# Optimization experiments

Measured on AMD Instinct MI355X. Metric: run time of the kernel, lower is better.

## Reference

```python
import jax, jax.numpy as jnp
import numpy as np

ALPHA = 0.25
GAMMA = 2.0
VAR0, VAR1 = 0.1, 0.2  # torch.Tensor([0.1, 0.2]) variances in encode
EPS = 1e-4


def _center_size(boxes):
    # corner (x1,y1,x2,y2) -> center (cx,cy,w,h)
    return jnp.concatenate([(boxes[:, :2] + boxes[:, 2:]) * 0.5,
                            boxes[:, 2:] - boxes[:, :2]], axis=1)


def _jaccard(a, b):
    # a: [A,4] anchors, b: [T,4] targets, corner form -> IoU [A,T]
    lt = jnp.maximum(a[:, None, :2], b[None, :, :2])
    rb = jnp.minimum(a[:, None, 2:], b[None, :, 2:])
    wh = jnp.clip(rb - lt, 0.0)
    inter = wh[..., 0] * wh[..., 1]
    area_a = (a[:, 2] - a[:, 0]) * (a[:, 3] - a[:, 1])
    area_b = (b[:, 2] - b[:, 0]) * (b[:, 3] - b[:, 1])
    return inter / (area_a[:, None] + area_b[None, :] - inter)


def _encode(matched, priors_cf):
    # matched: corner form [P,4]; priors_cf: center form [P,4]
    g_cxcy = ((matched[:, :2] + matched[:, 2:]) * 0.5 - priors_cf[:, :2]) / (VAR0 * priors_cf[:, 2:])
    g_wh = jnp.log((matched[:, 2:] - matched[:, :2]) / priors_cf[:, 2:]) / VAR1
    return jnp.concatenate([g_cxcy, g_wh], axis=1)


def _per_image(cla, reg, target, anchor, anchor_cf):
    # cla [A,C], reg [A,4], target [T,5]
    valid = target[:, 4] != -1.0                      # padded targets (label -1) are excluded
    has_valid = jnp.any(valid)
    cla = jnp.clip(cla, EPS, 1.0 - EPS)
    iou = _jaccard(anchor, target[:, :4])             # [A,T]
    iou = jnp.where(valid[None, :], iou, -1.0)        # mask padded targets (valid IoUs are >= 0)
    iou_argmax = jnp.argmax(iou, axis=1)              # [A]
    iou_max = jnp.take_along_axis(iou, iou_argmax[:, None], axis=1)[:, 0]
    pos = iou_max >= 0.5
    num_pos = jnp.sum(pos)
    assigned = target[iou_argmax]                     # [A,5] gather of matched gt

    C = cla.shape[1]
    onehot = jax.nn.one_hot(assigned[:, 4].astype(jnp.int32), C, dtype=cla.dtype)
    labels = jnp.full_like(cla, -1.0)
    labels = jnp.where(iou_max[:, None] < 0.4, 0.0, labels)
    labels = jnp.where(pos[:, None], onehot, labels)

    is_one = labels == 1.0
    alpha_factor = jnp.where(is_one, ALPHA, 1.0 - ALPHA)
    focal_weight = alpha_factor * jnp.where(is_one, 1.0 - cla, cla) ** GAMMA
    bce = -(labels * jnp.log(cla) + (1.0 - labels) * jnp.log1p(-cla))
    cls_loss = jnp.where(labels != -1.0, focal_weight * bce, 0.0)
    cls_loss = cls_loss.sum() / jnp.maximum(num_pos.astype(cla.dtype), 1.0)

    # smooth-L1 on positive anchors only; original takes .mean() over [P,4]
    enc_gt = _encode(assigned[:, :4], anchor_cf)      # [A,4]
    diff = jnp.abs(enc_gt - reg)
    sl1 = jnp.where(diff <= 1.0 / 9.0, 0.5 * 9.0 * diff * diff, diff - 0.5 / 9.0)
    denom = jnp.maximum(num_pos * 4, 1).astype(cla.dtype)
    reg_loss = jnp.where(num_pos > 0, jnp.sum(sl1 * pos[:, None]) / denom, 0.0)

    cls_loss = jnp.where(has_valid, cls_loss, 0.0)
    reg_loss = jnp.where(has_valid, reg_loss, 0.0)
    return cls_loss, reg_loss


def setup_inputs() -> dict:
    key = jax.random.key(0)
    ks = jax.random.split(key, 7)
    B, A, C, T = 8, 100000, 80, 50
    clas = jax.random.uniform(ks[0], (B, A, C), jnp.float32, 0.01, 0.99)
    regs = jax.random.normal(ks[1], (B, A, 4), jnp.float32)
    # anchors: valid corner boxes inside a ~1024x1024 image
    axy = jax.random.uniform(ks[2], (1, A, 2), jnp.float32, 0.0, 900.0)
    awh = jax.random.uniform(ks[3], (1, A, 2), jnp.float32, 16.0, 120.0)
    anchors = jnp.concatenate([axy, axy + awh], axis=-1)
    # targets: valid gt boxes with class id in [0, C) stored as float in column 4
    txy = jax.random.uniform(ks[4], (B, T, 2), jnp.float32, 0.0, 800.0)
    twh = jax.random.uniform(ks[5], (B, T, 2), jnp.float32, 20.0, 220.0)
    lab = jax.random.randint(ks[6], (B, T, 1), 0, C).astype(jnp.float32)
    targets = jnp.concatenate([txy, txy + twh, lab], axis=-1)
    return {"clas": clas, "regs": regs, "anchors": anchors, "targets": targets}


def reference(clas, regs, anchors, targets):
    anchor = anchors[0]                               # [A,4]
    anchor_cf = _center_size(anchor)
    cls_l, reg_l = jax.vmap(_per_image, in_axes=(0, 0, 0, None, None))(
        clas, regs, targets, anchor, anchor_cf)
    return (jnp.mean(cls_l, keepdims=True), jnp.mean(reg_l, keepdims=True))
```

## Files before the change

### kernel.cpp

```cpp
#include <hip/hip_runtime.h>

#define A_COUNT 100000
#define B_COUNT 8
#define C_COUNT 80
#define T_COUNT 50
#define BLOCK   256
#define NF4     (C_COUNT / 4)
#define FULL4   (BLOCK * NF4)

typedef float f4v __attribute__((ext_vector_type(4)));

__global__ __launch_bounds__(BLOCK) void retina_main(
    const float* __restrict__ clas,
    const float* __restrict__ regs,
    const float* __restrict__ anchors,
    const float* __restrict__ targets,
    float* __restrict__ ws_cls,
    float* __restrict__ ws_reg,
    int*   __restrict__ ws_pos)
{
    __shared__ float s_tgt[T_COUNT * 5];
    __shared__ int   s_state[BLOCK];
    __shared__ float s_c[4], s_r[4];
    __shared__ int   s_p[4];

    const int b    = blockIdx.y;
    const int base = blockIdx.x * BLOCK;
    const int tid  = threadIdx.x;

    for (int i = tid; i < T_COUNT * 5; i += BLOCK)
        s_tgt[i] = targets[b * T_COUNT * 5 + i];
    __syncthreads();

    const int a = base + tid;
    int   state  = -1;
    float my_reg = 0.0f;
    bool  my_pos = false;

    if (a < A_COUNT) {
        const float4 an = ((const float4*)anchors)[a];
        const float area_a = (an.z - an.x) * (an.w - an.y);

        float best = -1.0f;
        int   bestIdx = 0;
        bool  anyValid = false;

        #pragma unroll 1
        for (int t = 0; t < T_COUNT; ++t) {
            const float tx1 = s_tgt[t * 5 + 0];
            const float ty1 = s_tgt[t * 5 + 1];
            const float tx2 = s_tgt[t * 5 + 2];
            const float ty2 = s_tgt[t * 5 + 3];
            const float lab = s_tgt[t * 5 + 4];
            float iou = -1.0f;
            if (lab != -1.0f) {
                anyValid = true;
                const float lx = fmaxf(an.x, tx1), ly = fmaxf(an.y, ty1);
                const float rx = fminf(an.z, tx2), ry = fminf(an.w, ty2);
                const float w = fmaxf(rx - lx, 0.0f);
                const float h = fmaxf(ry - ly, 0.0f);
                const float inter  = w * h;
                const float area_b = (tx2 - tx1) * (ty2 - ty1);
                iou = inter / (area_a + area_b - inter);
            }
            if (iou > best) { best = iou; bestIdx = t; }
        }

        if (anyValid) {
            if (best >= 0.5f) {
                state  = (int)s_tgt[bestIdx * 5 + 4];
                my_pos = true;
                const float4 rg = ((const float4*)regs)[(size_t)b * A_COUNT + a];
                const float tx1 = s_tgt[bestIdx * 5 + 0];
                const float ty1 = s_tgt[bestIdx * 5 + 1];
                const float tx2 = s_tgt[bestIdx * 5 + 2];
                const float ty2 = s_tgt[bestIdx * 5 + 3];
                const float pcx = (an.x + an.z) * 0.5f, pcy = (an.y + an.w) * 0.5f;
                const float pw  = an.z - an.x,          ph  = an.w - an.y;
                const float mcx = (tx1 + tx2) * 0.5f,   mcy = (ty1 + ty2) * 0.5f;
                const float mw  = tx2 - tx1,            mh  = ty2 - ty1;
                const float e0 = (mcx - pcx) / (0.1f * pw);
                const float e1 = (mcy - pcy) / (0.1f * ph);
                const float e2 = __logf(mw / pw) * 5.0f;
                const float e3 = __logf(mh / ph) * 5.0f;
                const float d0 = fabsf(e0 - rg.x);
                const float d1 = fabsf(e1 - rg.y);
                const float d2 = fabsf(e2 - rg.z);
                const float d3 = fabsf(e3 - rg.w);
                const float th = 1.0f / 9.0f;
                const float c59 = 0.5f / 9.0f;
                const float s0 = (d0 <= th) ? 4.5f * d0 * d0 : d0 - c59;
                const float s1 = (d1 <= th) ? 4.5f * d1 * d1 : d1 - c59;
                const float s2 = (d2 <= th) ? 4.5f * d2 * d2 : d2 - c59;
                const float s3 = (d3 <= th) ? 4.5f * d3 * d3 : d3 - c59;
                my_reg = s0 + s1 + s2 + s3;
            } else if (best < 0.4f) {
                state = 128;
            }
        }
    }
    s_state[tid] = state;
    __syncthreads();

    const int nA = min(BLOCK, A_COUNT - base);
    const f4v* cl4 = (const f4v*)(clas + ((size_t)b * A_COUNT + base) * C_COUNT);
    float cls_local = 0.0f;

    if (nA == BLOCK) {
        int aL = tid / NF4;
        int cL = tid - aL * NF4;
        #pragma unroll
        for (int ko = 0; ko < 5; ++ko) {
            f4v v[4];
            #pragma unroll
            for (int u = 0; u < 4; ++u)
                v[u] = __builtin_nontemporal_load(&cl4[tid + (ko * 4 + u) * BLOCK]);
            #pragma unroll
            for (int u = 0; u < 4; ++u) {
                const int st  = s_state[aL];
                const float w = (st == -1) ? 0.0f : 0.75f;
                #pragma unroll
                for (int j = 0; j < 4; ++j) {
                    float p = fminf(fmaxf(v[u][j], 1e-4f), 1.0f - 1e-4f);
                    float l = __logf(1.0f - p);
                    cls_local = fmaf(p * p * l, -w, cls_local);
                }
                aL += 12; cL += 16;
                if (cL >= NF4) { cL -= NF4; ++aL; }
            }
        }
    } else {
        const int count4 = nA * NF4;
        for (int i = tid; i < count4; i += BLOCK) {
            const int st = s_state[i / NF4];
            if (st == -1) continue;
            const f4v v = __builtin_nontemporal_load(&cl4[i]);
            #pragma unroll
            for (int j = 0; j < 4; ++j) {
                float p = fminf(fmaxf(v[j], 1e-4f), 1.0f - 1e-4f);
                float l = __logf(1.0f - p);
                cls_local = fmaf(p * p * l, -0.75f, cls_local);
            }
        }
    }

    if (my_pos) {
        float p = clas[((size_t)b * A_COUNT + a) * C_COUNT + state];
        p = fminf(fmaxf(p, 1e-4f), 1.0f - 1e-4f);
        const float om = 1.0f - p;
        cls_local += 0.25f * om * om * (-__logf(p))
                   - 0.75f * p * p * (-__logf(om));
    }

    float r0 = cls_local, r1 = my_reg;
    const unsigned long long bal = __ballot(my_pos);
    const int posc = __popcll(bal);
    #pragma unroll
    for (int off = 32; off > 0; off >>= 1) {
        r0 += __shfl_down(r0, off);
        r1 += __shfl_down(r1, off);
    }
    const int wave = tid >> 6, lane = tid & 63;
    if (lane == 0) { s_c[wave] = r0; s_r[wave] = r1; s_p[wave] = posc; }
    __syncthreads();
    if (tid == 0) {
        float tc = 0.0f, tr = 0.0f; int tp = 0;
        #pragma unroll
        for (int w = 0; w < 4; ++w) { tc += s_c[w]; tr += s_r[w]; tp += s_p[w]; }
        atomicAdd(&ws_cls[b], tc);
        atomicAdd(&ws_reg[b], tr);
        atomicAdd(&ws_pos[b], tp);
    }
}

__global__ void retina_final(const float* __restrict__ ws_cls,
                             const float* __restrict__ ws_reg,
                             const int*   __restrict__ ws_pos,
                             float* __restrict__ out)
{
    const int tid = threadIdx.x;
    float cl = 0.0f, rl = 0.0f;
    if (tid < B_COUNT) {
        const int   npi = ws_pos[tid];
        const float np  = (float)npi;
        cl = ws_cls[tid] / fmaxf(np, 1.0f);
        rl = (npi > 0) ? ws_reg[tid] / (np * 4.0f) : 0.0f;
    }
    #pragma unroll
    for (int off = 4; off > 0; off >>= 1) {
        cl += __shfl_down(cl, off);
        rl += __shfl_down(rl, off);
    }
    if (tid == 0) {
        out[0] = cl * (1.0f / (float)B_COUNT);
        out[1] = rl * (1.0f / (float)B_COUNT);
    }
}

extern "C" void kernel_launch(void* const* d_in, const int* in_sizes, int n_in,
                              void* d_out, int out_size, void* d_ws, size_t ws_size,
                              hipStream_t stream) {
    const float* clas    = (const float*)d_in[0];
    const float* regs    = (const float*)d_in[1];
    const float* anchors = (const float*)d_in[2];
    const float* targets = (const float*)d_in[3];

    float* ws_cls = (float*)d_ws;
    float* ws_reg = ws_cls + B_COUNT;
    int*   ws_pos = (int*)(ws_reg + B_COUNT);

    hipMemsetAsync(d_ws, 0, (2 * B_COUNT) * sizeof(float) + B_COUNT * sizeof(int), stream);

    dim3 grid((A_COUNT + BLOCK - 1) / BLOCK, B_COUNT);
    retina_main<<<grid, BLOCK, 0, stream>>>(clas, regs, anchors, targets,
                                            ws_cls, ws_reg, ws_pos);
    retina_final<<<1, 64, 0, stream>>>(ws_cls, ws_reg, ws_pos, (float*)d_out);
}
```

Before: 405.2 us.

## Prefetch class tiles before IoU matching and software-pipeline the focal-loss loads

Issues the first four nontemporal loads of the block's class-probability tile before the anchor–target IoU matching runs, then streams the remaining loads through an 8-slot register ring with a lookahead of four. The goal is to hide DRAM latency behind the matching compute. The shared-memory target staging and its barrier are removed, so targets are read straight from global memory with uniform addresses. The IoU loop is now branchless and partially unrolled. Costs are higher register pressure from the ring buffer, and the out-of-range anchor index is clamped so every lane can run the loop.

New measurement: 399.6 us. Within noise of the previous version (-1.4%).

```diff
diff --git a/kernel.cpp b/kernel.cpp
--- a/kernel.cpp
+++ b/kernel.cpp
@@ -19,7 +19,6 @@
     float* __restrict__ ws_reg,
     int*   __restrict__ ws_pos)
 {
-    __shared__ float s_tgt[T_COUNT * 5];
     __shared__ int   s_state[BLOCK];
     __shared__ float s_c[4], s_r[4];
     __shared__ int   s_p[4];
@@ -27,107 +26,108 @@
     const int b    = blockIdx.y;
     const int base = blockIdx.x * BLOCK;
     const int tid  = threadIdx.x;
-
-    for (int i = tid; i < T_COUNT * 5; i += BLOCK)
-        s_tgt[i] = targets[b * T_COUNT * 5 + i];
-    __syncthreads();
-
-    const int a = base + tid;
+    const int a    = base + tid;
+    const int nA   = min(BLOCK, A_COUNT - base);
+    const bool full = (nA == BLOCK);
+
+    const f4v* cl4 = (const f4v*)(clas + ((size_t)b * A_COUNT + base) * C_COUNT);
+
+    f4v buf[8];
+    if (full) {
+        #pragma unroll
+        for (int u = 0; u < 4; ++u)
+            buf[u] = __builtin_nontemporal_load(&cl4[tid + u * BLOCK]);
+    }
+
+    const float* tgt = targets + b * T_COUNT * 5;
+
+    const int ac = min(a, A_COUNT - 1);
+    const float4 an = ((const float4*)anchors)[ac];
+    const float area_a = (an.z - an.x) * (an.w - an.y);
+
+    float best = -1.0f;
+    int   bestIdx = 0;
+    bool  anyValid = false;
+
+    #pragma unroll 5
+    for (int t = 0; t < T_COUNT; ++t) {
+        const float tx1 = tgt[t * 5 + 0];
+        const float ty1 = tgt[t * 5 + 1];
+        const float tx2 = tgt[t * 5 + 2];
+        const float ty2 = tgt[t * 5 + 3];
+        const float lab = tgt[t * 5 + 4];
+        const bool valid = (lab != -1.0f);
+        anyValid |= valid;
+        const float lx = fmaxf(an.x, tx1), ly = fmaxf(an.y, ty1);
+        const float rx = fminf(an.z, tx2), ry = fminf(an.w, ty2);
+        const float w = fmaxf(rx - lx, 0.0f);
+        const float h = fmaxf(ry - ly, 0.0f);
+        const float inter  = w * h;
+        const float area_b = (tx2 - tx1) * (ty2 - ty1);
+        float iou = inter / (area_a + area_b - inter);
+        iou = valid ? iou : -1.0f;
+        if (iou > best) { best = iou; bestIdx = t; }
+    }
+
     int   state  = -1;
     float my_reg = 0.0f;
     bool  my_pos = false;
 
-    if (a < A_COUNT) {
-        const float4 an = ((const float4*)anchors)[a];
-        const float area_a = (an.z - an.x) * (an.w - an.y);
-
-        float best = -1.0f;
-        int   bestIdx = 0;
-        bool  anyValid = false;
-
-        #pragma unroll 1
-        for (int t = 0; t < T_COUNT; ++t) {
-            const float tx1 = s_tgt[t * 5 + 0];
-            const float ty1 = s_tgt[t * 5 + 1];
-            const float tx2 = s_tgt[t * 5 + 2];
-            const float ty2 = s_tgt[t * 5 + 3];
-            const float lab = s_tgt[t * 5 + 4];
-            float iou = -1.0f;
-            if (lab != -1.0f) {
-                anyValid = true;
-                const float lx = fmaxf(an.x, tx1), ly = fmaxf(an.y, ty1);
-                const float rx = fminf(an.z, tx2), ry = fminf(an.w, ty2);
-                const float w = fmaxf(rx - lx, 0.0f);
-                const float h = fmaxf(ry - ly, 0.0f);
-                const float inter  = w * h;
-                const float area_b = (tx2 - tx1) * (ty2 - ty1);
-                iou = inter / (area_a + area_b - inter);
-            }
-            if (iou > best) { best = iou; bestIdx = t; }
-        }
-
-        if (anyValid) {
-            if (best >= 0.5f) {
-                state  = (int)s_tgt[bestIdx * 5 + 4];
-                my_pos = true;
-                const float4 rg = ((const float4*)regs)[(size_t)b * A_COUNT + a];
-                const float tx1 = s_tgt[bestIdx * 5 + 0];
-                const float ty1 = s_tgt[bestIdx * 5 + 1];
-                const float tx2 = s_tgt[bestIdx * 5 + 2];
-                const float ty2 = s_tgt[bestIdx * 5 + 3];
-                const float pcx = (an.x + an.z) * 0.5f, pcy = (an.y + an.w) * 0.5f;
-                const float pw  = an.z - an.x,          ph  = an.w - an.y;
-                const float mcx = (tx1 + tx2) * 0.5f,   mcy = (ty1 + ty2) * 0.5f;
-                const float mw  = tx2 - tx1,            mh  = ty2 - ty1;
-                const float e0 = (mcx - pcx) / (0.1f * pw);
-                const float e1 = (mcy - pcy) / (0.1f * ph);
-                const float e2 = __logf(mw / pw) * 5.0f;
-                const float e3 = __logf(mh / ph) * 5.0f;
-                const float d0 = fabsf(e0 - rg.x);
-                const float d1 = fabsf(e1 - rg.y);
-                const float d2 = fabsf(e2 - rg.z);
-                const float d3 = fabsf(e3 - rg.w);
-                const float th = 1.0f / 9.0f;
-                const float c59 = 0.5f / 9.0f;
-                const float s0 = (d0 <= th) ? 4.5f * d0 * d0 : d0 - c59;
-                const float s1 = (d1 <= th) ? 4.5f * d1 * d1 : d1 - c59;
-                const float s2 = (d2 <= th) ? 4.5f * d2 * d2 : d2 - c59;
-                const float s3 = (d3 <= th) ? 4.5f * d3 * d3 : d3 - c59;
-                my_reg = s0 + s1 + s2 + s3;
-            } else if (best < 0.4f) {
-                state = 128;
-            }
+    if (a < A_COUNT && anyValid) {
+        if (best >= 0.5f) {
+            const float tx1 = tgt[bestIdx * 5 + 0];
+            const float ty1 = tgt[bestIdx * 5 + 1];
+            const float tx2 = tgt[bestIdx * 5 + 2];
+            const float ty2 = tgt[bestIdx * 5 + 3];
+            state  = (int)tgt[bestIdx * 5 + 4];
+            my_pos = true;
+            const float4 rg = ((const float4*)regs)[(size_t)b * A_COUNT + a];
+            const float pcx = (an.x + an.z) * 0.5f, pcy = (an.y + an.w) * 0.5f;
+            const float pw  = an.z - an.x,          ph  = an.w - an.y;
+            const float mcx = (tx1 + tx2) * 0.5f,   mcy = (ty1 + ty2) * 0.5f;
+            const float mw  = tx2 - tx1,            mh  = ty2 - ty1;
+            const float e0 = (mcx - pcx) / (0.1f * pw);
+            const float e1 = (mcy - pcy) / (0.1f * ph);
+            const float e2 = __logf(mw / pw) * 5.0f;
+            const float e3 = __logf(mh / ph) * 5.0f;
+            const float d0 = fabsf(e0 - rg.x);
+            const float d1 = fabsf(e1 - rg.y);
+            const float d2 = fabsf(e2 - rg.z);
+            const float d3 = fabsf(e3 - rg.w);
+            const float th = 1.0f / 9.0f;
+            const float c59 = 0.5f / 9.0f;
+            const float s0 = (d0 <= th) ? 4.5f * d0 * d0 : d0 - c59;
+            const float s1 = (d1 <= th) ? 4.5f * d1 * d1 : d1 - c59;
+            const float s2 = (d2 <= th) ? 4.5f * d2 * d2 : d2 - c59;
+            const float s3 = (d3 <= th) ? 4.5f * d3 * d3 : d3 - c59;
+            my_reg = s0 + s1 + s2 + s3;
+        } else if (best < 0.4f) {
+            state = 128;
         }
     }
     s_state[tid] = state;
     __syncthreads();
 
-    const int nA = min(BLOCK, A_COUNT - base);
-    const f4v* cl4 = (const f4v*)(clas + ((size_t)b * A_COUNT + base) * C_COUNT);
     float cls_local = 0.0f;
 
-    if (nA == BLOCK) {
+    if (full) {
         int aL = tid / NF4;
         int cL = tid - aL * NF4;
         #pragma unroll
-        for (int ko = 0; ko < 5; ++ko) {
-            f4v v[4];
+        for (int i = 0; i < 20; ++i) {
+            if (i + 4 < 20)
+                buf[(i + 4) & 7] = __builtin_nontemporal_load(&cl4[tid + (i + 4) * BLOCK]);
+            const f4v v = buf[i & 7];
+            const int st  = s_state[aL];
+            const float w = (st == -1) ? 0.0f : 0.75f;
             #pragma unroll
-            for (int u = 0; u < 4; ++u)
-                v[u] = __builtin_nontemporal_load(&cl4[tid + (ko * 4 + u) * BLOCK]);
-            #pragma unroll
-            for (int u = 0; u < 4; ++u) {
-                const int st  = s_state[aL];
-                const float w = (st == -1) ? 0.0f : 0.75f;
-                #pragma unroll
-                for (int j = 0; j < 4; ++j) {
-                    float p = fminf(fmaxf(v[u][j], 1e-4f), 1.0f - 1e-4f);
-                    float l = __logf(1.0f - p);
-                    cls_local = fmaf(p * p * l, -w, cls_local);
-                }
-                aL += 12; cL += 16;
-                if (cL >= NF4) { cL -= NF4; ++aL; }
+            for (int j = 0; j < 4; ++j) {
+                float p = fminf(fmaxf(v[j], 1e-4f), 1.0f - 1e-4f);
+                float l = __logf(1.0f - p);
+                cls_local = fmaf(p * p * l, -w, cls_local);
             }
+            aL += 12; cL += 16;
+            if (cL >= NF4) { cL -= NF4; ++aL; }
         }
     } else {
         const int count4 = nA * NF4;
```
